# Kernel optimization log

Hardware: AMD Instinct MI355X
Metric: run time of the kernel (lower is better)

## Reference

```python
import math
import jax, jax.numpy as jnp
import numpy as np

B, A, U, S, E, HYP, H = 16384, 32, 64, 2048, 32, 64, 4
ATTEND_REG_COEF = 1e-3


def setup_inputs() -> dict:
    key = jax.random.key(0)
    ks = jax.random.split(key, 12)
    sc = 0.05
    return {
        "agent_qs": jax.random.normal(ks[0], (B, A), jnp.float32),
        "states": jax.random.normal(ks[1], (B, S), jnp.float32),
        # per-head selector hypernet: Linear(S,HYP)+ReLU+Linear(HYP,E,no bias)
        "sel_w1": jax.random.normal(ks[2], (H, S, HYP), jnp.float32) * sc,
        "sel_b1": jax.random.normal(ks[3], (H, HYP), jnp.float32) * sc,
        "sel_w2": jax.random.normal(ks[4], (H, HYP, E), jnp.float32) * sc,
        # per-head key extractor: Linear(U,E,no bias)
        "key_w": jax.random.normal(ks[5], (H, U, E), jnp.float32) * sc,
        # V net: Linear(S,E)+ReLU+Linear(E,1)
        "v_w1": jax.random.normal(ks[6], (S, E), jnp.float32) * sc,
        "v_b1": jax.random.normal(ks[7], (E,), jnp.float32) * sc,
        "v_w2": jax.random.normal(ks[8], (E, 1), jnp.float32) * sc,
        "v_b2": jax.random.normal(ks[9], (1,), jnp.float32) * sc,
    }


def reference(agent_qs, states, sel_w1, sel_b1, sel_w2, key_w, v_w1, v_b1, v_w2, v_b2):
    # nonlinear=False, weighted_head=False, state_bias=True (defaults used here)
    unit_states = states[:, : A * U].reshape(-1, A, U)  # [B, A, U]

    # per-head selectors: [B, H, E]
    h1 = jax.nn.relu(jnp.einsum("bs,hsk->bhk", states, sel_w1) + sel_b1[None])
    selectors = jnp.einsum("bhk,hke->bhe", h1, sel_w2)

    # per-head, per-agent keys: [B, H, A, E]
    keys = jnp.einsum("bau,hue->bhae", unit_states, key_w)

    # attention logits [B, H, A] (matches selector @ stacked-keys in torch)
    logits = jnp.einsum("bhe,bhae->bha", selectors, keys)
    weights = jax.nn.softmax(logits / math.sqrt(E), axis=-1)  # [B, H, A]

    head_attend = jnp.sum(weights, axis=1)  # [B, A]

    v = jax.nn.relu(states @ v_w1 + v_b1) @ v_w2 + v_b2  # [B, 1]

    # coef * sum over heads of mean(logits_h ** 2)
    attend_mag_regs = ATTEND_REG_COEF * jnp.sum(jnp.mean(logits ** 2, axis=(0, 2)))

    # per-head entropy: -(p * log(p + 1e-8)).sum(agents).mean(batch) -> [H]
    head_entropies = -jnp.mean(
        jnp.sum(weights * jnp.log(weights + 1e-8), axis=-1), axis=0
    )

    return head_attend, v, attend_mag_regs, head_entropies
```

## Files before the change

kernel.cpp:

```cpp
#include <hip/hip_runtime.h>
#include <hip/hip_bf16.h>

#define B_N 16384
#define A_N 32
#define U_N 64
#define S_N 2048
#define E_N 32
#define HYP_N 64
#define H_N 4
#define NREAL 288
#define NPADG 320

#define WS_WT    0
#define WS_MB    1310720
#define WS_PMAG  (WS_MB + 32768)
#define WS_PENT  (WS_PMAG + 65536)

#define OUT_V   (B_N * A_N)
#define OUT_MAG (OUT_V + B_N)
#define OUT_ENT (OUT_MAG + 1)

typedef __attribute__((ext_vector_type(8))) short bf16x8_t;
typedef __attribute__((ext_vector_type(4))) float floatx4_t;

#define AS1(p) ((const __attribute__((address_space(1))) void*)(p))
#define AS3(p) ((__attribute__((address_space(3))) void*)(p))

__device__ __forceinline__ unsigned short f2b(float f) {
    union { float f; unsigned u; } v; v.f = f;
    unsigned r = v.u + 0x7FFFu + ((v.u >> 16) & 1u);
    return (unsigned short)(r >> 16);
}
__device__ __forceinline__ float b2f(unsigned x) {
    union { unsigned u; float f; } v; v.u = x << 16; return v.f;
}

__global__ __launch_bounds__(256) void pack_w_kernel(
        const float* __restrict__ sel_w1, const float* __restrict__ v_w1,
        const float* __restrict__ sel_w2, const float* __restrict__ key_w,
        unsigned short* __restrict__ Wt, unsigned short* __restrict__ Mb) {
    int idx = blockIdx.x * 256 + threadIdx.x;
    if (idx < NPADG * S_N) {
        int n = idx >> 11;
        int k = idx & 2047;
        float val = 0.0f;
        if (n < 256) {
            int h = n >> 6, kk = n & 63;
            val = sel_w1[((size_t)h * S_N + k) * HYP_N + kk];
        } else if (n < NREAL) {
            val = v_w1[(size_t)k * E_N + (n - 256)];
        }
        Wt[idx] = f2b(val);
    } else if (idx < NPADG * S_N + H_N * U_N * HYP_N) {
        int j = idx - NPADG * S_N;
        int h = j >> 12, u = (j >> 6) & 63, k = j & 63;
        const float* kw = key_w + ((size_t)h * U_N + u) * E_N;
        const float* w2 = sel_w2 + ((size_t)h * HYP_N + k) * E_N;
        float s = 0.0f;
#pragma unroll
        for (int e = 0; e < E_N; ++e) s = fmaf(kw[e], w2[e], s);
        Mb[j] = f2b(s);
    }
}

#define FM_BM 32
#define FM_BK 64
#define NIT   (S_N / FM_BK)
#define H1_STRIDE 312
#define TS_STRIDE 260

__global__ __launch_bounds__(512, 4) void fused_kernel(
        const float* __restrict__ states, const unsigned short* __restrict__ Wt,
        const float* __restrict__ sel_b1, const float* __restrict__ v_b1,
        const unsigned short* __restrict__ Mb,
        const float* __restrict__ v_w2, const float* __restrict__ v_b2,
        float* __restrict__ out, float* __restrict__ pmag, float* __restrict__ pent) {
    __shared__ __align__(16) char pool[4096 + 40960 + H1_STRIDE * FM_BM * 2];
    unsigned short* Asm = (unsigned short*)pool;
    unsigned short* Bsm = (unsigned short*)(pool + 4096);
    float*          tsb = (float*)(pool + 4096);
    unsigned short* h1b = (unsigned short*)(pool + 4096 + 40960);

    const int t = threadIdx.x;
    const int lane = t & 63;
    const int w = t >> 6;
    const int m0 = blockIdx.x * FM_BM;
    const int miw = (w & 1) * 16;
    const int nw = (w >> 1) * 80;

    const int ar = t >> 3, acl = t & 7;
    const float* ap = states + (size_t)(m0 + ar) * S_N + acl * 8;

    floatx4_t acc[5] = {};
    float4 a0, a1;

    if (t < 256) {
        a0 = *(const float4*)(ap);
        a1 = *(const float4*)(ap + 4);
        int ph = acl ^ (ar & 7);
        uint4 o;
        o.x = (unsigned)f2b(a0.x) | ((unsigned)f2b(a0.y) << 16);
        o.y = (unsigned)f2b(a0.z) | ((unsigned)f2b(a0.w) << 16);
        o.z = (unsigned)f2b(a1.x) | ((unsigned)f2b(a1.y) << 16);
        o.w = (unsigned)f2b(a1.z) | ((unsigned)f2b(a1.w) << 16);
        *(uint4*)(Asm + (size_t)(ar * 8 + ph) * 8) = o;
    }
#pragma unroll
    for (int i = 0; i < 5; ++i) {
        int p = i * 512 + t, n = p >> 3, sl = p & 7;
        int cl = sl ^ (n & 7);
        __builtin_amdgcn_global_load_lds(AS1(Wt + (size_t)n * S_N + cl * 8),
                                         AS3(Bsm + p * 8), 16, 0, 0);
    }
    if (t < 256) {
        a0 = *(const float4*)(ap + FM_BK);
        a1 = *(const float4*)(ap + FM_BK + 4);
    }
    __syncthreads();

    for (int it = 0; it < NIT; ++it) {
#pragma unroll
        for (int s = 0; s < 2; ++s) {
            const int c = s * 4 + (lane >> 4);
            int r = miw + (lane & 15);
            int pha = c ^ (r & 7);
            bf16x8_t afr = *(const bf16x8_t*)(Asm + r * 64 + pha * 8);
#pragma unroll
            for (int nt = 0; nt < 5; ++nt) {
                int n = nw + nt * 16 + (lane & 15);
                int ph = c ^ (n & 7);
                bf16x8_t bfr = *(const bf16x8_t*)(Bsm + n * 64 + ph * 8);
                acc[nt] = __builtin_amdgcn_mfma_f32_16x16x32_bf16(
                    afr, bfr, acc[nt], 0, 0, 0);
            }
        }
        __syncthreads();
        if (it < NIT - 1) {
            int k0 = (it + 1) * FM_BK;
            if (t < 256) {
                int ph = acl ^ (ar & 7);
                uint4 o;
                o.x = (unsigned)f2b(a0.x) | ((unsigned)f2b(a0.y) << 16);
                o.y = (unsigned)f2b(a0.z) | ((unsigned)f2b(a0.w) << 16);
                o.z = (unsigned)f2b(a1.x) | ((unsigned)f2b(a1.y) << 16);
                o.w = (unsigned)f2b(a1.z) | ((unsigned)f2b(a1.w) << 16);
                *(uint4*)(Asm + (size_t)(ar * 8 + ph) * 8) = o;
            }
#pragma unroll
            for (int i = 0; i < 5; ++i) {
                int p = i * 512 + t, n = p >> 3, sl = p & 7;
                int cl = sl ^ (n & 7);
                __builtin_amdgcn_global_load_lds(
                    AS1(Wt + (size_t)n * S_N + k0 + cl * 8),
                    AS3(Bsm + p * 8), 16, 0, 0);
            }
            if (it < NIT - 2 && t < 256) {
                const float* g = ap + (it + 2) * FM_BK;
                a0 = *(const float4*)(g);
                a1 = *(const float4*)(g + 4);
            }
            __syncthreads();
        }
    }

#pragma unroll
    for (int nt = 0; nt < 5; ++nt) {
        int n = nw + nt * 16 + (lane & 15);
        if (n >= NREAL) continue;
        float bias = (n < 256) ? sel_b1[n] : v_b1[n - 256];
        int slot = (n < 256) ? ((n >> 6) * 72 + (n & 63))
                             : (((n - 256) >> 3) * 72 + 64 + ((n - 256) & 7));
#pragma unroll
        for (int rg = 0; rg < 4; ++rg) {
            int r = miw + (lane >> 4) * 4 + rg;
            float v = acc[nt][rg] + bias;
            h1b[r * H1_STRIDE + slot] = f2b(v > 0.0f ? v : 0.0f);
        }
    }
    __syncthreads();

    {
        const int h = w >> 1;
        const int rb = (w & 1) * 16;
        floatx4_t tacc[4] = {};
#pragma unroll
        for (int s = 0; s < 2; ++s) {
            int k0 = s * 32 + (lane >> 4) * 8;
            bf16x8_t afr = *(const bf16x8_t*)(h1b + (rb + (lane & 15)) * H1_STRIDE
                                              + h * 72 + k0);
#pragma unroll
            for (int ut = 0; ut < 4; ++ut) {
                int u = ut * 16 + (lane & 15);
                bf16x8_t bfr = *(const bf16x8_t*)(Mb + ((size_t)(h * U_N + u) * 64) + k0);
                tacc[ut] = __builtin_amdgcn_mfma_f32_16x16x32_bf16(
                    afr, bfr, tacc[ut], 0, 0, 0);
            }
        }
#pragma unroll
        for (int ut = 0; ut < 4; ++ut)
#pragma unroll
            for (int rg = 0; rg < 4; ++rg) {
                int r = rb + (lane >> 4) * 4 + rg;
                int u = ut * 16 + (lane & 15);
                tsb[r * TS_STRIDE + h * U_N + u] = tacc[ut][rg];
            }
    }
    __syncthreads();

    const int a = lane & 31, uh = lane >> 5;
    float4 cur[8], nxt[8];
    {
        const float* up = states + (size_t)(m0 + w * 4) * S_N + a * 64 + uh * 32;
#pragma unroll
        for (int i = 0; i < 8; ++i) cur[i] = ((const float4*)up)[i];
    }
    for (int rr = 0; rr < 4; ++rr) {
        int r = w * 4 + rr;
        int b = m0 + r;
        if (rr < 3) {
            const float* up = states + (size_t)(b + 1) * S_N + a * 64 + uh * 32;
#pragma unroll
            for (int i = 0; i < 8; ++i) nxt[i] = ((const float4*)up)[i];
        }
        float pl[4];
#pragma unroll
        for (int h = 0; h < 4; ++h) {
            const float* tp = &tsb[r * TS_STRIDE + h * U_N + uh * 32];
            float s = 0.0f;
#pragma unroll
            for (int i = 0; i < 8; ++i) {
                float4 t4 = *(const float4*)(tp + i * 4);
                s = fmaf(cur[i].x, t4.x, s);
                s = fmaf(cur[i].y, t4.y, s);
                s = fmaf(cur[i].z, t4.z, s);
                s = fmaf(cur[i].w, t4.w, s);
            }
            pl[h] = s + __shfl_xor(s, 32, 64);
        }
        float mg = pl[0]*pl[0] + pl[1]*pl[1] + pl[2]*pl[2] + pl[3]*pl[3];
#pragma unroll
        for (int o = 16; o > 0; o >>= 1) mg += __shfl_xor(mg, o, 32);
        float hatt = 0.0f;
        float entv[4];
#pragma unroll
        for (int h = 0; h < 4; ++h) {
            float x = pl[h] * 0.17677669529663687f;
            float m = x;
#pragma unroll
            for (int o = 16; o > 0; o >>= 1) m = fmaxf(m, __shfl_xor(m, o, 32));
            float p = expf(x - m);
            float den = p;
#pragma unroll
            for (int o = 16; o > 0; o >>= 1) den += __shfl_xor(den, o, 32);
            float wv = p / den;
            hatt += wv;
            float e = wv * logf(wv + 1e-8f);
#pragma unroll
            for (int o = 16; o > 0; o >>= 1) e += __shfl_xor(e, o, 32);
            entv[h] = e;
        }
        if (uh == 0) {
            out[(size_t)b * A_N + a] = hatt;
            float pv = b2f((unsigned)h1b[r * H1_STRIDE + (a >> 3) * 72 + 64 + (a & 7)])
                       * v_w2[a];
#pragma unroll
            for (int o = 16; o > 0; o >>= 1) pv += __shfl_xor(pv, o, 32);
            if (a == 0) {
                out[OUT_V + b] = pv + v_b2[0];
                pmag[b] = mg;
#pragma unroll
                for (int h = 0; h < 4; ++h) pent[(size_t)h * B_N + b] = entv[h];
            }
        }
#pragma unroll
        for (int i = 0; i < 8; ++i) cur[i] = nxt[i];
    }
}

__global__ __launch_bounds__(256) void finalize_kernel(
        const float* __restrict__ pmag, const float* __restrict__ pent,
        float* __restrict__ out) {
    int which = blockIdx.x;
    const float* src = (which == 0) ? pmag : (pent + (size_t)(which - 1) * B_N);
    float s = 0.0f;
    for (int i = threadIdx.x; i < B_N; i += 256) s += src[i];
#pragma unroll
    for (int o = 32; o > 0; o >>= 1) s += __shfl_xor(s, o, 64);
    __shared__ float red[4];
    if ((threadIdx.x & 63) == 0) red[threadIdx.x >> 6] = s;
    __syncthreads();
    if (threadIdx.x == 0) {
        float tot = red[0] + red[1] + red[2] + red[3];
        if (which == 0) out[OUT_MAG] = 1e-3f * tot / (float)(B_N * A_N);
        else out[OUT_ENT + which - 1] = -tot / (float)B_N;
    }
}

extern "C" void kernel_launch(void* const* d_in, const int* in_sizes, int n_in,
                              void* d_out, int out_size, void* d_ws, size_t ws_size,
                              hipStream_t stream) {
    const float* states = (const float*)d_in[1];
    const float* sel_w1 = (const float*)d_in[2];
    const float* sel_b1 = (const float*)d_in[3];
    const float* sel_w2 = (const float*)d_in[4];
    const float* key_w  = (const float*)d_in[5];
    const float* v_w1   = (const float*)d_in[6];
    const float* v_b1   = (const float*)d_in[7];
    const float* v_w2   = (const float*)d_in[8];
    const float* v_b2   = (const float*)d_in[9];
    float* out = (float*)d_out;
    char* wsb  = (char*)d_ws;

    unsigned short* Wt  = (unsigned short*)(wsb + WS_WT);
    unsigned short* Mb  = (unsigned short*)(wsb + WS_MB);
    float* pmag         = (float*)(wsb + WS_PMAG);
    float* pent         = (float*)(wsb + WS_PENT);

    pack_w_kernel<<<dim3((NPADG * S_N + H_N * U_N * HYP_N + 255) / 256),
                    dim3(256), 0, stream>>>(sel_w1, v_w1, sel_w2, key_w, Wt, Mb);
    fused_kernel<<<dim3(B_N / FM_BM), dim3(512), 0, stream>>>(
        states, Wt, sel_b1, v_b1, Mb, v_w2, v_b2, out, pmag, pent);
    finalize_kernel<<<dim3(5), dim3(256), 0, stream>>>(pmag, pent, out);
}
```

Before: 280.0 us.

## Split fused kernel into GEMM-h1 and attention kernels with global h1 buffer

Splits the single fused kernel into a GEMM kernel that writes relu(h1) as bf16 to a workspace buffer and a separate attention kernel that computes per-head logits, softmax, entropy and V from that buffer. Dropping the h1 and ts buffers from the GEMM kernel's shared memory and raising its occupancy bound are meant to allow more blocks per CU, and the attention kernel uses smaller blocks. The softmax drops the max subtraction, uses fast __expf/__logf, and computes entropy in closed form as sum(p*x)/den - log(den). The costs are an extra launch, a global round trip for h1 of about 10MB, and a risk of overflow or precision change from the unstabilised softmax.

```diff
diff --git a/kernel.cpp b/kernel.cpp
--- a/kernel.cpp
+++ b/kernel.cpp
@@ -11,10 +11,14 @@
 #define NREAL 288
 #define NPADG 320
 
+#define H1_STRIDE 312
+#define TS_STRIDE 260
+
 #define WS_WT    0
 #define WS_MB    1310720
 #define WS_PMAG  (WS_MB + 32768)
 #define WS_PENT  (WS_PMAG + 65536)
+#define WS_H1    (WS_PENT + 262144)
 
 #define OUT_V   (B_N * A_N)
 #define OUT_MAG (OUT_V + B_N)
@@ -30,9 +34,6 @@
     union { float f; unsigned u; } v; v.f = f;
     unsigned r = v.u + 0x7FFFu + ((v.u >> 16) & 1u);
     return (unsigned short)(r >> 16);
-}
-__device__ __forceinline__ float b2f(unsigned x) {
-    union { unsigned u; float f; } v; v.u = x << 16; return v.f;
 }
 
 __global__ __launch_bounds__(256) void pack_w_kernel(
@@ -66,20 +67,14 @@
 #define FM_BM 32
 #define FM_BK 64
 #define NIT   (S_N / FM_BK)
-#define H1_STRIDE 312
-#define TS_STRIDE 260
-
-__global__ __launch_bounds__(512, 4) void fused_kernel(
+
+__global__ __launch_bounds__(512, 6) void gemm_h1_kernel(
         const float* __restrict__ states, const unsigned short* __restrict__ Wt,
         const float* __restrict__ sel_b1, const float* __restrict__ v_b1,
-        const unsigned short* __restrict__ Mb,
-        const float* __restrict__ v_w2, const float* __restrict__ v_b2,
-        float* __restrict__ out, float* __restrict__ pmag, float* __restrict__ pent) {
-    __shared__ __align__(16) char pool[4096 + 40960 + H1_STRIDE * FM_BM * 2];
+        unsigned short* __restrict__ h1g) {
+    __shared__ __align__(16) char pool[4096 + 40960];
     unsigned short* Asm = (unsigned short*)pool;
     unsigned short* Bsm = (unsigned short*)(pool + 4096);
-    float*          tsb = (float*)(pool + 4096);
-    unsigned short* h1b = (unsigned short*)(pool + 4096 + 40960);
 
     const int t = threadIdx.x;
     const int lane = t & 63;
@@ -163,6 +158,7 @@
         }
     }
 
+    unsigned short* hrow = h1g + (size_t)m0 * H1_STRIDE;
 #pragma unroll
     for (int nt = 0; nt < 5; ++nt) {
         int n = nw + nt * 16 + (lane & 15);
@@ -174,20 +170,33 @@
         for (int rg = 0; rg < 4; ++rg) {
             int r = miw + (lane >> 4) * 4 + rg;
             float v = acc[nt][rg] + bias;
-            h1b[r * H1_STRIDE + slot] = f2b(v > 0.0f ? v : 0.0f);
-        }
-    }
-    __syncthreads();
+            hrow[(size_t)r * H1_STRIDE + slot] = f2b(v > 0.0f ? v : 0.0f);
+        }
+    }
+}
+
+#define K2_BM 16
+
+__global__ __launch_bounds__(256, 8) void attend_kernel(
+        const float* __restrict__ states, const unsigned short* __restrict__ h1g,
+        const unsigned short* __restrict__ Mb,
+        const float* __restrict__ v_w2, const float* __restrict__ v_b2,
+        float* __restrict__ out, float* __restrict__ pmag, float* __restrict__ pent) {
+    __shared__ __align__(16) float tsb[K2_BM * TS_STRIDE];
+    const int t = threadIdx.x;
+    const int lane = t & 63;
+    const int w = t >> 6;
+    const int m0 = blockIdx.x * K2_BM;
 
     {
-        const int h = w >> 1;
-        const int rb = (w & 1) * 16;
+        const int h = w;
+        const unsigned short* hbase =
+            h1g + (size_t)(m0 + (lane & 15)) * H1_STRIDE + h * 72;
         floatx4_t tacc[4] = {};
 #pragma unroll
         for (int s = 0; s < 2; ++s) {
             int k0 = s * 32 + (lane >> 4) * 8;
-            bf16x8_t afr = *(const bf16x8_t*)(h1b + (rb + (lane & 15)) * H1_STRIDE
-                                              + h * 72 + k0);
+            bf16x8_t afr = *(const bf16x8_t*)(hbase + k0);
 #pragma unroll
             for (int ut = 0; ut < 4; ++ut) {
                 int u = ut * 16 + (lane & 15);
@@ -200,7 +209,7 @@
         for (int ut = 0; ut < 4; ++ut)
 #pragma unroll
             for (int rg = 0; rg < 4; ++rg) {
-                int r = rb + (lane >> 4) * 4 + rg;
+                int r = (lane >> 4) * 4 + rg;
                 int u = ut * 16 + (lane & 15);
                 tsb[r * TS_STRIDE + h * U_N + u] = tacc[ut][rg];
             }
@@ -208,61 +217,58 @@
     __syncthreads();
 
     const int a = lane & 31, uh = lane >> 5;
-    float4 cur[8], nxt[8];
-    {
-        const float* up = states + (size_t)(m0 + w * 4) * S_N + a * 64 + uh * 32;
-#pragma unroll
-        for (int i = 0; i < 8; ++i) cur[i] = ((const float4*)up)[i];
-    }
     for (int rr = 0; rr < 4; ++rr) {
-        int r = w * 4 + rr;
-        int b = m0 + r;
-        if (rr < 3) {
-            const float* up = states + (size_t)(b + 1) * S_N + a * 64 + uh * 32;
-#pragma unroll
-            for (int i = 0; i < 8; ++i) nxt[i] = ((const float4*)up)[i];
-        }
-        float pl[4];
-#pragma unroll
-        for (int h = 0; h < 4; ++h) {
-            const float* tp = &tsb[r * TS_STRIDE + h * U_N + uh * 32];
-            float s = 0.0f;
-#pragma unroll
-            for (int i = 0; i < 8; ++i) {
-                float4 t4 = *(const float4*)(tp + i * 4);
-                s = fmaf(cur[i].x, t4.x, s);
-                s = fmaf(cur[i].y, t4.y, s);
-                s = fmaf(cur[i].z, t4.z, s);
-                s = fmaf(cur[i].w, t4.w, s);
-            }
-            pl[h] = s + __shfl_xor(s, 32, 64);
-        }
+        const int r = w * 4 + rr;
+        const int b = m0 + r;
+        const float* up = states + (size_t)b * S_N + a * 64 + uh * 32;
+        const float* tp = &tsb[r * TS_STRIDE + uh * 32];
+        float pl[4] = {0.0f, 0.0f, 0.0f, 0.0f};
+        float4 c0 = ((const float4*)up)[0];
+        float4 c1 = ((const float4*)up)[1];
+#pragma unroll
+        for (int i = 0; i < 8; ++i) {
+            float4 s4 = c0;
+            c0 = c1;
+            if (i < 6) c1 = ((const float4*)up)[i + 2];
+#pragma unroll
+            for (int h = 0; h < 4; ++h) {
+                float4 t4 = *(const float4*)(tp + h * U_N + i * 4);
+                pl[h] = fmaf(s4.x, t4.x, pl[h]);
+                pl[h] = fmaf(s4.y, t4.y, pl[h]);
+                pl[h] = fmaf(s4.z, t4.z, pl[h]);
+                pl[h] = fmaf(s4.w, t4.w, pl[h]);
+            }
+        }
+#pragma unroll
+        for (int h = 0; h < 4; ++h)
+            pl[h] += __shfl_xor(pl[h], 32, 64);
+
         float mg = pl[0]*pl[0] + pl[1]*pl[1] + pl[2]*pl[2] + pl[3]*pl[3];
 #pragma unroll
         for (int o = 16; o > 0; o >>= 1) mg += __shfl_xor(mg, o, 32);
+
         float hatt = 0.0f;
         float entv[4];
 #pragma unroll
         for (int h = 0; h < 4; ++h) {
             float x = pl[h] * 0.17677669529663687f;
-            float m = x;
-#pragma unroll
-            for (int o = 16; o > 0; o >>= 1) m = fmaxf(m, __shfl_xor(m, o, 32));
-            float p = expf(x - m);
-            float den = p;
-#pragma unroll
-            for (int o = 16; o > 0; o >>= 1) den += __shfl_xor(den, o, 32);
-            float wv = p / den;
-            hatt += wv;
-            float e = wv * logf(wv + 1e-8f);
-#pragma unroll
-            for (int o = 16; o > 0; o >>= 1) e += __shfl_xor(e, o, 32);
-            entv[h] = e;
-        }
+            float p = __expf(x);
+            float den = p, px = p * x;
+#pragma unroll
+            for (int o = 16; o > 0; o >>= 1) {
+                den += __shfl_xor(den, o, 32);
+                px  += __shfl_xor(px,  o, 32);
+            }
+            float inv = 1.0f / den;
+            hatt = fmaf(p, inv, hatt);
+            entv[h] = px * inv - __logf(den);
+        }
+
         if (uh == 0) {
             out[(size_t)b * A_N + a] = hatt;
-            float pv = b2f((unsigned)h1b[r * H1_STRIDE + (a >> 3) * 72 + 64 + (a & 7)])
-                       * v_w2[a];
+            unsigned hv = h1g[(size_t)b * H1_STRIDE + (a >> 3) * 72 + 64 + (a & 7)];
+            union { unsigned u; float f; } cv; cv.u = hv << 16;
+            float pv = cv.f * v_w2[a];
 #pragma unroll
             for (int o = 16; o > 0; o >>= 1) pv += __shfl_xor(pv, o, 32);
             if (a == 0) {
@@ -272,8 +278,6 @@
                 for (int h = 0; h < 4; ++h) pent[(size_t)h * B_N + b] = entv[h];
             }
         }
-#pragma unroll
-        for (int i = 0; i < 8; ++i) cur[i] = nxt[i];
     }
 }
 
@@ -315,10 +319,13 @@
     unsigned short* Mb  = (unsigned short*)(wsb + WS_MB);
     float* pmag         = (float*)(wsb + WS_PMAG);
     float* pent         = (float*)(wsb + WS_PENT);
+    unsigned short* h1g = (unsigned short*)(wsb + WS_H1);
 
     pack_w_kernel<<<dim3((NPADG * S_N + H_N * U_N * HYP_N + 255) / 256),
                     dim3(256), 0, stream>>>(sel_w1, v_w1, sel_w2, key_w, Wt, Mb);
-    fused_kernel<<<dim3(B_N / FM_BM), dim3(512), 0, stream>>>(
-        states, Wt, sel_b1, v_b1, Mb, v_w2, v_b2, out, pmag, pent);
+    gemm_h1_kernel<<<dim3(B_N / FM_BM), dim3(512), 0, stream>>>(
+        states, Wt, sel_b1, v_b1, h1g);
+    attend_kernel<<<dim3(B_N / K2_BM), dim3(256), 0, stream>>>(
+        states, h1g, Mb, v_w2, v_b2, out, pmag, pent);
     finalize_kernel<<<dim3(5), dim3(256), 0, stream>>>(pmag, pent, out);
 }
```

After: 283.2 us. Within noise of the previous version (+1.1%).
